# Kernel tuning notes

Hardware: AMD Instinct MI355X
Metric: run time of the kernel (lower is better)

The kernel has to match this reference:

```python
import jax, jax.numpy as jnp
import numpy as np
import math

D_MODEL = 6144
N_HEADS = 48
N_KV_HEADS = 8
HEAD_DIM = D_MODEL // N_HEADS  # 128
ROPE_DIM = HEAD_DIM
ROPE_BASE = 500000.0
CLAMP = 8.0
B, T = 1, 2048


def _apply_rope(x, rope_dim, base):
    # x: [B, n, T, H]; rotate interleaved pairs in first rope_dim dims.
    b, n, t, h = x.shape
    rd = min(rope_dim, h)
    inv = 1.0 / base ** (jnp.arange(0, rd, 2, dtype=jnp.float32) / rd)  # [rd/2]
    pos = jnp.arange(t, dtype=jnp.float32)
    freqs = pos[:, None] * inv[None, :]            # [T, rd/2]
    cos = jnp.cos(freqs)[None, None]               # [1,1,T,rd/2]
    sin = jnp.sin(freqs)[None, None]
    x1 = x[..., :rd].reshape(b, n, t, rd // 2, 2)
    a, b2 = x1[..., 0], x1[..., 1]
    a2 = a * cos - b2 * sin
    b3 = a * sin + b2 * cos
    x1_out = jnp.stack([a2, b3], axis=-1).reshape(b, n, t, rd)
    return jnp.concatenate([x1_out, x[..., rd:]], axis=-1) if rd < h else x1_out


def setup_inputs() -> dict:
    key = jax.random.key(0)
    k1, k2, k3 = jax.random.split(key, 3)
    x = jax.random.normal(k1, (B, T, D_MODEL), dtype=jnp.float32)
    w_qkv = jax.random.normal(k2, (D_MODEL + 2 * N_KV_HEADS * HEAD_DIM, D_MODEL), dtype=jnp.float32) * 0.02
    w_out = jax.random.normal(k3, (D_MODEL, D_MODEL), dtype=jnp.float32) * 0.02
    # additive causal mask: 0 on/below diagonal, -1e9 above
    neg = jnp.full((T, T), -1e9, dtype=jnp.float32)
    causal_mask = jnp.triu(neg, k=1)[None, None]  # [1,1,T,T]
    return {"x": x, "causal_mask": causal_mask, "w_qkv": w_qkv, "w_out": w_out}


def reference(x, causal_mask, w_qkv, w_out):
    b, t, _ = x.shape
    qkv = jnp.einsum('btd,od->bto', x, w_qkv)  # [B,T,8192]
    kv_dim = N_KV_HEADS * HEAD_DIM
    q = qkv[..., :D_MODEL]
    k = qkv[..., D_MODEL:D_MODEL + kv_dim]
    v = qkv[..., D_MODEL + kv_dim:]
    # split heads -> [B, n, T, H]
    q = q.reshape(b, t, N_HEADS, HEAD_DIM).transpose(0, 2, 1, 3)
    k = k.reshape(b, t, N_KV_HEADS, HEAD_DIM).transpose(0, 2, 1, 3)
    v = v.reshape(b, t, N_KV_HEADS, HEAD_DIM).transpose(0, 2, 1, 3)
    q = _apply_rope(q, ROPE_DIM, ROPE_BASE)
    k = _apply_rope(k, ROPE_DIM, ROPE_BASE)
    q = jnp.clip(q, -CLAMP, CLAMP)
    k = jnp.clip(k, -CLAMP, CLAMP)
    v = jnp.clip(v, -CLAMP, CLAMP)
    rep = N_HEADS // N_KV_HEADS
    k = jnp.repeat(k, rep, axis=1)  # GQA repeat_kv -> [B, n_heads, T, H]
    v = jnp.repeat(v, rep, axis=1)
    scale = 1.0 / math.sqrt(HEAD_DIM)
    scores = jnp.einsum('bnqh,bnkh->bnqk', q, k) * scale
    scores = scores + causal_mask
    probs = jax.nn.softmax(scores.astype(jnp.float32), axis=-1).astype(x.dtype)
    attn = jnp.einsum('bnqk,bnkh->bnqh', probs, v)
    attn = attn.transpose(0, 2, 1, 3).reshape(b, t, D_MODEL)
    return jnp.einsum('btd,od->bto', attn, w_out)
```

## Files before the change

### kernel.cpp

```cpp
#include <hip/hip_runtime.h>


typedef __attribute__((ext_vector_type(8))) short bf16x8;
typedef __attribute__((ext_vector_type(4))) float f32x4;

__device__ inline short f2bf(float f) {
  union { float f; unsigned u; } v; v.f = f;
  unsigned r = v.u + 0x7fffu + ((v.u >> 16) & 1u);
  return (short)(r >> 16);
}

__global__ void cvt_bf16(const float* __restrict__ in, short* __restrict__ out, int n8) {
  int i = blockIdx.x * 256 + threadIdx.x;
  if (i >= n8) return;
  const float4* p = (const float4*)in;
  float4 a = p[2 * i], b = p[2 * i + 1];
  bf16x8 r;
  r[0] = f2bf(a.x); r[1] = f2bf(a.y); r[2] = f2bf(a.z); r[3] = f2bf(a.w);
  r[4] = f2bf(b.x); r[5] = f2bf(b.y); r[6] = f2bf(b.z); r[7] = f2bf(b.w);
  *((bf16x8*)out + i) = r;
}

__device__ inline void gload_lds16(const short* g, short* l) {
  __builtin_amdgcn_global_load_lds(
      (const __attribute__((address_space(1))) void*)g,
      (__attribute__((address_space(3))) void*)l, 16, 0, 0);
}

__global__ __launch_bounds__(256) void gemm_bt(const short* __restrict__ A,
                                               const short* __restrict__ B,
                                               float* __restrict__ C,
                                               int M, int N, int K) {
  __shared__ short As[128 * 32];
  __shared__ short Bs[128 * 32];
  int tid = threadIdx.x;
  int wave = tid >> 6, lane = tid & 63;
  int lm = lane & 15, quad = lane >> 4;
  int nwg = gridDim.x * gridDim.y;
  int wg = blockIdx.y * gridDim.x + blockIdx.x;
  int cpx = nwg >> 3;
  int swz = (wg & 7) * cpx + (wg >> 3);
  int bxi = swz % gridDim.x;
  int byi = swz / gridDim.x;
  int bm = byi * 128, bn = bxi * 128;
  int wm = (wave >> 1) * 64, wn = (wave & 1) * 64;
  f32x4 acc[4][4] = {};
  for (int k0 = 0; k0 < K; k0 += 32) {
#pragma unroll
    for (int i = 0; i < 2; ++i) {
      int c = tid + i * 256;
      gload_lds16(A + (size_t)(bm + (c >> 2)) * K + k0 + (c & 3) * 8,
                  As + (i * 256 + wave * 64) * 8);
    }
#pragma unroll
    for (int i = 0; i < 2; ++i) {
      int c = tid + i * 256;
      gload_lds16(B + (size_t)(bn + (c >> 2)) * K + k0 + (c & 3) * 8,
                  Bs + (i * 256 + wave * 64) * 8);
    }
    __syncthreads();
    bf16x8 a[4], b[4];
#pragma unroll
    for (int r = 0; r < 4; ++r)
      a[r] = *(const bf16x8*)(As + (wm + r * 16 + lm) * 32 + quad * 8);
#pragma unroll
    for (int c = 0; c < 4; ++c)
      b[c] = *(const bf16x8*)(Bs + (wn + c * 16 + lm) * 32 + quad * 8);
#pragma unroll
    for (int r = 0; r < 4; ++r)
#pragma unroll
      for (int c = 0; c < 4; ++c)
        acc[r][c] = __builtin_amdgcn_mfma_f32_16x16x32_bf16(a[r], b[c], acc[r][c], 0, 0, 0);
    __syncthreads();
  }
#pragma unroll
  for (int r = 0; r < 4; ++r)
#pragma unroll
    for (int c = 0; c < 4; ++c)
#pragma unroll
      for (int e = 0; e < 4; ++e)
        C[(size_t)(bm + wm + r * 16 + quad * 4 + e) * N + (bn + wn + c * 16 + lm)] =
            acc[r][c][e];
}

__global__ void rope_split(const float* __restrict__ qkv, short* __restrict__ Qb,
                           short* __restrict__ Kb, short* __restrict__ Vtb) {
  int idx = blockIdx.x * 256 + threadIdx.x;
  int t = idx >> 12;
  int p = idx & 4095;
  int o = p * 2;
  float2 ab = *(const float2*)(qkv + (size_t)t * 8192 + o);
  float a = ab.x, b = ab.y;
  if (o < 7168) {
    int d = o & 127;
    float ang = (float)t * exp2f((float)d * (-18.931568569324174f / 128.0f));
    float s, c;
    sincosf(ang, &s, &c);
    float a2 = a * c - b * s;
    float b2 = a * s + b * c;
    a = a2; b = b2;
  }
  a = fminf(8.0f, fmaxf(-8.0f, a));
  b = fminf(8.0f, fmaxf(-8.0f, b));
  short sa = f2bf(a), sb = f2bf(b);
  if (o < 6144) {
    int h = o >> 7, d = o & 127;
    short* q = Qb + (size_t)(h * 2048 + t) * 128 + d;
    q[0] = sa; q[1] = sb;
  } else if (o < 7168) {
    int oo = o - 6144; int h = oo >> 7, d = oo & 127;
    short* k = Kb + (size_t)(h * 2048 + t) * 128 + d;
    k[0] = sa; k[1] = sb;
  } else {
    int oo = o - 7168; int h = oo >> 7, d = oo & 127;
    Vtb[(size_t)(h * 128 + d) * 2048 + t]     = sa;
    Vtb[(size_t)(h * 128 + d + 1) * 2048 + t] = sb;
  }
}

__global__ __launch_bounds__(256) void flash_attn(const short* __restrict__ Q,
                                                  const short* __restrict__ K,
                                                  const short* __restrict__ Vt,
                                                  short* __restrict__ Ob) {
  __shared__ short Ks[64 * 136];
  __shared__ short Vs[128 * 72];
  __shared__ short Ps[4][16 * 72];
  int bid = blockIdx.x;
  int mtile = 31 - (bid / 48);
  int h = bid % 48;
  int hk = h / 6;
  int tid = threadIdx.x, wave = tid >> 6, lane = tid & 63;
  int lm = lane & 15, quad = lane >> 4;
  int qrow0 = mtile * 64 + wave * 16;
  bf16x8 qf[4];
#pragma unroll
  for (int kc = 0; kc < 4; ++kc)
    qf[kc] = *(const bf16x8*)(Q + (size_t)(h * 2048 + qrow0 + lm) * 128 + kc * 32 + quad * 8);
  const short* gk[4]; short* lk[4];
  const short* gv[4]; short* lv[4];
#pragma unroll
  for (int i = 0; i < 4; ++i) {
    int c = tid + i * 256;
    int r = c >> 4, ko = (c & 15) * 8;
    gk[i] = K + (size_t)(hk * 2048 + r) * 128 + ko;
    lk[i] = Ks + r * 136 + ko;
    int d = c >> 3, to = (c & 7) * 8;
    gv[i] = Vt + (size_t)(hk * 128 + d) * 2048 + to;
    lv[i] = Vs + d * 72 + to;
  }
  f32x4 o_acc[8] = {};
  float m_run[4] = {-1e30f, -1e30f, -1e30f, -1e30f};
  float l_run[4] = {0.f, 0.f, 0.f, 0.f};
  const float sc = 0.08838834764831845f;
  int nkv = mtile + 1;
  bf16x8 kst[4], vst[4];
#pragma unroll
  for (int i = 0; i < 4; ++i) {
    kst[i] = *(const bf16x8*)(gk[i]);
    vst[i] = *(const bf16x8*)(gv[i]);
  }
  for (int kb = 0; kb < nkv; ++kb) {
    int kv0 = kb * 64;
    __syncthreads();
#pragma unroll
    for (int i = 0; i < 4; ++i) {
      *(bf16x8*)lk[i] = kst[i];
      *(bf16x8*)lv[i] = vst[i];
    }
    __syncthreads();
    if (kb + 1 < nkv) {
      int kv1 = kv0 + 64;
#pragma unroll
      for (int i = 0; i < 4; ++i) {
        kst[i] = *(const bf16x8*)(gk[i] + (size_t)kv1 * 128);
        vst[i] = *(const bf16x8*)(gv[i] + kv1);
      }
    }
    f32x4 s[4];
    __builtin_amdgcn_s_setprio(1);
#pragma unroll
    for (int ct = 0; ct < 4; ++ct) {
      f32x4 acc = {};
#pragma unroll
      for (int kc = 0; kc < 4; ++kc) {
        bf16x8 bfr = *(const bf16x8*)(Ks + (ct * 16 + lm) * 136 + kc * 32 + quad * 8);
        acc = __builtin_amdgcn_mfma_f32_16x16x32_bf16(qf[kc], bfr, acc, 0, 0, 0);
      }
      s[ct] = acc;
    }
    __builtin_amdgcn_s_setprio(0);
#pragma unroll
    for (int ct = 0; ct < 4; ++ct)
#pragma unroll
      for (int e = 0; e < 4; ++e) s[ct][e] *= sc;
    if (kb == mtile) {
#pragma unroll
      for (int ct = 0; ct < 4; ++ct) {
        int col = kv0 + ct * 16 + lm;
#pragma unroll
        for (int e = 0; e < 4; ++e) {
          int row = qrow0 + quad * 4 + e;
          if (col > row) s[ct][e] = -1e30f;
        }
      }
    }
    float mx[4];
#pragma unroll
    for (int e = 0; e < 4; ++e)
      mx[e] = fmaxf(fmaxf(s[0][e], s[1][e]), fmaxf(s[2][e], s[3][e]));
#pragma unroll
    for (int off = 1; off < 16; off <<= 1)
#pragma unroll
      for (int e = 0; e < 4; ++e) mx[e] = fmaxf(mx[e], __shfl_xor(mx[e], off, 64));
    float alpha[4];
#pragma unroll
    for (int e = 0; e < 4; ++e) {
      float mn = fmaxf(m_run[e], mx[e]);
      alpha[e] = __expf(m_run[e] - mn);
      m_run[e] = mn;
    }
    float rs[4] = {0.f, 0.f, 0.f, 0.f};
#pragma unroll
    for (int ct = 0; ct < 4; ++ct)
#pragma unroll
      for (int e = 0; e < 4; ++e) {
        float pv = __expf(s[ct][e] - m_run[e]);
        s[ct][e] = pv;
        rs[e] += pv;
      }
#pragma unroll
    for (int off = 1; off < 16; off <<= 1)
#pragma unroll
      for (int e = 0; e < 4; ++e) rs[e] += __shfl_xor(rs[e], off, 64);
#pragma unroll
    for (int e = 0; e < 4; ++e) l_run[e] = l_run[e] * alpha[e] + rs[e];
#pragma unroll
    for (int ot = 0; ot < 8; ++ot)
#pragma unroll
      for (int e = 0; e < 4; ++e) o_acc[ot][e] *= alpha[e];
    short* pw = &Ps[wave][0];
#pragma unroll
    for (int ct = 0; ct < 4; ++ct)
#pragma unroll
      for (int e = 0; e < 4; ++e)
        pw[(quad * 4 + e) * 72 + ct * 16 + lm] = f2bf(s[ct][e]);
    __builtin_amdgcn_s_setprio(1);
#pragma unroll
    for (int kc = 0; kc < 2; ++kc) {
      bf16x8 afr = *(const bf16x8*)(pw + lm * 72 + kc * 32 + quad * 8);
#pragma unroll
      for (int ot = 0; ot < 8; ++ot) {
        bf16x8 bfr = *(const bf16x8*)(Vs + (ot * 16 + lm) * 72 + kc * 32 + quad * 8);
        o_acc[ot] = __builtin_amdgcn_mfma_f32_16x16x32_bf16(afr, bfr, o_acc[ot], 0, 0, 0);
      }
    }
    __builtin_amdgcn_s_setprio(0);
  }
#pragma unroll
  for (int ot = 0; ot < 8; ++ot)
#pragma unroll
    for (int e = 0; e < 4; ++e) {
      float v = o_acc[ot][e] / l_run[e];
      Ob[(size_t)(qrow0 + quad * 4 + e) * 6144 + h * 128 + ot * 16 + lm] = f2bf(v);
    }
}

extern "C" void kernel_launch(void* const* d_in, const int* in_sizes, int n_in,
                              void* d_out, int out_size, void* d_ws, size_t ws_size,
                              hipStream_t stream) {
  const float* x     = (const float*)d_in[0];
  const float* w_qkv = (const float*)d_in[2];
  const float* w_out = (const float*)d_in[3];
  float* out = (float*)d_out;

  short* xb    = (short*)d_ws;
  short* wqkvb = xb + (size_t)2048 * 6144;
  short* woutb = wqkvb + (size_t)8192 * 6144;
  float* qkvf  = (float*)(woutb + (size_t)6144 * 6144);
  short* Qb    = (short*)(qkvf + (size_t)2048 * 8192);
  short* Kb    = Qb + (size_t)48 * 2048 * 128;
  short* Vtb   = Kb + (size_t)8 * 2048 * 128;
  short* attnb = Vtb + (size_t)8 * 128 * 2048;

  cvt_bf16<<<(2048 * 6144 / 8) / 256, 256, 0, stream>>>(x, xb, 2048 * 6144 / 8);
  cvt_bf16<<<(8192 * 6144 / 8) / 256, 256, 0, stream>>>(w_qkv, wqkvb, 8192 * 6144 / 8);
  cvt_bf16<<<(6144 * 6144 / 8) / 256, 256, 0, stream>>>(w_out, woutb, 6144 * 6144 / 8);

  gemm_bt<<<dim3(8192 / 128, 2048 / 128), 256, 0, stream>>>(xb, wqkvb, qkvf, 2048, 8192, 6144);

  rope_split<<<(2048 * 4096) / 256, 256, 0, stream>>>(qkvf, Qb, Kb, Vtb);

  flash_attn<<<dim3(1536), 256, 0, stream>>>(Qb, Kb, Vtb, attnb);

  gemm_bt<<<dim3(6144 / 128, 2048 / 128), 256, 0, stream>>>(attnb, woutb, out, 2048, 6144, 6144);
}
```

Before: 1.196 ms.

## Replace GEMM with 256x128 triple-buffered swizzled-LDS pipelined kernel

Swaps the simple 128x128 single-buffered GEMM (K-step 32, two syncthreads per step) for a 256x128 tile kernel with 512 threads, K-step 64 and three LDS buffers. Global-to-LDS loads are issued two tiles ahead, overlapping with the MFMAs. LDS rows are XOR-swizzled to avoid bank conflicts, and s_setprio and sched_barrier pin the schedule. The aim is to hide memory latency and raise MFMA utilisation in both projection GEMMs. The cost is 144KB of dynamic LDS (so 2 blocks/CU is unlikely to fit) and hand-written vmcnt waits that must match the issue order exactly.

```diff
diff --git a/kernel.cpp b/kernel.cpp
--- a/kernel.cpp
+++ b/kernel.cpp
@@ -21,66 +21,147 @@
   *((bf16x8*)out + i) = r;
 }
 
-__device__ inline void gload_lds16(const short* g, short* l) {
+__device__ __forceinline__ void gload_lds16(const short* g, short* l) {
   __builtin_amdgcn_global_load_lds(
       (const __attribute__((address_space(1))) void*)g,
       (__attribute__((address_space(3))) void*)l, 16, 0, 0);
 }
 
-__global__ __launch_bounds__(256) void gemm_bt(const short* __restrict__ A,
-                                               const short* __restrict__ B,
-                                               float* __restrict__ C,
-                                               int M, int N, int K) {
-  __shared__ short As[128 * 32];
-  __shared__ short Bs[128 * 32];
+__device__ __forceinline__ bf16x8 frag_ld(const short* buf, int row, int kb) {
+  int off = row * 128 + (kb ^ ((row & 7) << 4));
+  return *(const bf16x8*)((const char*)buf + off);
+}
+
+__device__ __forceinline__ void pin_barrier() {
+  asm volatile("" ::: "memory");
+  __builtin_amdgcn_sched_barrier(0);
+  __builtin_amdgcn_s_barrier();
+  __builtin_amdgcn_sched_barrier(0);
+}
+
+__device__ __forceinline__ void gemm_tile(
+    int t, int nt, const short* Ac, const short* Bc, short* Asg, short* Bsg,
+    const short* const srcA[4], const int ldsoA[4],
+    const short* const srcB[2], const int ldsoB[2],
+    int wm, int wn, int lm, int quad, f32x4 acc[4][4]) {
+  const bool stage = (t + 2 < nt);
+  const int koff = (t + 2) << 6;
+  bf16x8 a[2][2], b[4][2];
+#pragma unroll
+  for (int fr = 0; fr < 2; ++fr)
+#pragma unroll
+    for (int ks = 0; ks < 2; ++ks)
+      a[fr][ks] = frag_ld(Ac, wm * 64 + fr * 16 + lm, ks * 64 + quad * 16);
+#pragma unroll
+  for (int fc = 0; fc < 4; ++fc)
+#pragma unroll
+    for (int ks = 0; ks < 2; ++ks)
+      b[fc][ks] = frag_ld(Bc, wn * 64 + fc * 16 + lm, ks * 64 + quad * 16);
+  if (stage) {
+#pragma unroll
+    for (int i = 0; i < 4; ++i) gload_lds16(srcA[i] + koff, Asg + ldsoA[i]);
+  }
+  pin_barrier();
+  __builtin_amdgcn_s_setprio(1);
+#pragma unroll
+  for (int fr = 0; fr < 2; ++fr)
+#pragma unroll
+    for (int fc = 0; fc < 4; ++fc) {
+      acc[fr][fc] = __builtin_amdgcn_mfma_f32_16x16x32_bf16(a[fr][0], b[fc][0], acc[fr][fc], 0, 0, 0);
+      acc[fr][fc] = __builtin_amdgcn_mfma_f32_16x16x32_bf16(a[fr][1], b[fc][1], acc[fr][fc], 0, 0, 0);
+    }
+  __builtin_amdgcn_s_setprio(0);
+  pin_barrier();
+  bf16x8 a2[2][2];
+#pragma unroll
+  for (int fr = 0; fr < 2; ++fr)
+#pragma unroll
+    for (int ks = 0; ks < 2; ++ks)
+      a2[fr][ks] = frag_ld(Ac, wm * 64 + (fr + 2) * 16 + lm, ks * 64 + quad * 16);
+  if (stage) {
+#pragma unroll
+    for (int i = 0; i < 2; ++i) gload_lds16(srcB[i] + koff, Bsg + ldsoB[i]);
+    asm volatile("s_waitcnt vmcnt(6)" ::: "memory");
+  } else {
+    asm volatile("s_waitcnt vmcnt(0)" ::: "memory");
+  }
+  pin_barrier();
+  __builtin_amdgcn_s_setprio(1);
+#pragma unroll
+  for (int fr = 0; fr < 2; ++fr)
+#pragma unroll
+    for (int fc = 0; fc < 4; ++fc) {
+      acc[fr + 2][fc] = __builtin_amdgcn_mfma_f32_16x16x32_bf16(a2[fr][0], b[fc][0], acc[fr + 2][fc], 0, 0, 0);
+      acc[fr + 2][fc] = __builtin_amdgcn_mfma_f32_16x16x32_bf16(a2[fr][1], b[fc][1], acc[fr + 2][fc], 0, 0, 0);
+    }
+  __builtin_amdgcn_s_setprio(0);
+  pin_barrier();
+}
+
+__global__ __launch_bounds__(512, 2) void gemm256(const short* __restrict__ A,
+                                                  const short* __restrict__ B,
+                                                  float* __restrict__ C,
+                                                  int M, int N, int K) {
+  extern __shared__ short lds[];
+  short* const A0 = lds;
+  short* const A1 = lds + 16384;
+  short* const A2 = lds + 32768;
+  short* const B0 = lds + 49152;
+  short* const B1 = lds + 57344;
+  short* const B2 = lds + 65536;
   int tid = threadIdx.x;
   int wave = tid >> 6, lane = tid & 63;
   int lm = lane & 15, quad = lane >> 4;
+  int wm = wave >> 1, wn = wave & 1;
   int nwg = gridDim.x * gridDim.y;
   int wg = blockIdx.y * gridDim.x + blockIdx.x;
   int cpx = nwg >> 3;
   int swz = (wg & 7) * cpx + (wg >> 3);
-  int bxi = swz % gridDim.x;
-  int byi = swz / gridDim.x;
-  int bm = byi * 128, bn = bxi * 128;
-  int wm = (wave >> 1) * 64, wn = (wave & 1) * 64;
+  int bn = (swz % gridDim.x) * 128;
+  int bm = (swz / gridDim.x) * 256;
+  int nt = K >> 6;
+  const short* srcA[4]; int ldsoA[4];
+#pragma unroll
+  for (int i = 0; i < 4; ++i) {
+    int c = i * 512 + tid;
+    int row = c >> 3, kc = (c & 7) ^ (row & 7);
+    srcA[i] = A + (size_t)(bm + row) * K + kc * 8;
+    ldsoA[i] = c * 8;
+  }
+  const short* srcB[2]; int ldsoB[2];
+#pragma unroll
+  for (int i = 0; i < 2; ++i) {
+    int c = i * 512 + tid;
+    int row = c >> 3, kc = (c & 7) ^ (row & 7);
+    srcB[i] = B + (size_t)(bn + row) * K + kc * 8;
+    ldsoB[i] = c * 8;
+  }
+#pragma unroll
+  for (int i = 0; i < 4; ++i) gload_lds16(srcA[i], A0 + ldsoA[i]);
+#pragma unroll
+  for (int i = 0; i < 2; ++i) gload_lds16(srcB[i], B0 + ldsoB[i]);
+#pragma unroll
+  for (int i = 0; i < 4; ++i) gload_lds16(srcA[i] + 64, A1 + ldsoA[i]);
+#pragma unroll
+  for (int i = 0; i < 2; ++i) gload_lds16(srcB[i] + 64, B1 + ldsoB[i]);
+  asm volatile("s_waitcnt vmcnt(6)" ::: "memory");
+  __builtin_amdgcn_s_barrier();
+  __builtin_amdgcn_sched_barrier(0);
+
   f32x4 acc[4][4] = {};
-  for (int k0 = 0; k0 < K; k0 += 32) {
-#pragma unroll
-    for (int i = 0; i < 2; ++i) {
-      int c = tid + i * 256;
-      gload_lds16(A + (size_t)(bm + (c >> 2)) * K + k0 + (c & 3) * 8,
-                  As + (i * 256 + wave * 64) * 8);
-    }
-#pragma unroll
-    for (int i = 0; i < 2; ++i) {
-      int c = tid + i * 256;
-      gload_lds16(B + (size_t)(bn + (c >> 2)) * K + k0 + (c & 3) * 8,
-                  Bs + (i * 256 + wave * 64) * 8);
-    }
-    __syncthreads();
-    bf16x8 a[4], b[4];
-#pragma unroll
-    for (int r = 0; r < 4; ++r)
-      a[r] = *(const bf16x8*)(As + (wm + r * 16 + lm) * 32 + quad * 8);
-#pragma unroll
-    for (int c = 0; c < 4; ++c)
-      b[c] = *(const bf16x8*)(Bs + (wn + c * 16 + lm) * 32 + quad * 8);
-#pragma unroll
-    for (int r = 0; r < 4; ++r)
-#pragma unroll
-      for (int c = 0; c < 4; ++c)
-        acc[r][c] = __builtin_amdgcn_mfma_f32_16x16x32_bf16(a[r], b[c], acc[r][c], 0, 0, 0);
-    __syncthreads();
-  }
-#pragma unroll
-  for (int r = 0; r < 4; ++r)
-#pragma unroll
-    for (int c = 0; c < 4; ++c)
+  for (int t = 0; t < nt; t += 3) {
+    gemm_tile(t,     nt, A0, B0, A2, B2, srcA, ldsoA, srcB, ldsoB, wm, wn, lm, quad, acc);
+    gemm_tile(t + 1, nt, A1, B1, A0, B0, srcA, ldsoA, srcB, ldsoB, wm, wn, lm, quad, acc);
+    gemm_tile(t + 2, nt, A2, B2, A1, B1, srcA, ldsoA, srcB, ldsoB, wm, wn, lm, quad, acc);
+  }
+#pragma unroll
+  for (int fr = 0; fr < 4; ++fr)
+#pragma unroll
+    for (int fc = 0; fc < 4; ++fc)
 #pragma unroll
       for (int e = 0; e < 4; ++e)
-        C[(size_t)(bm + wm + r * 16 + quad * 4 + e) * N + (bn + wn + c * 16 + lm)] =
-            acc[r][c][e];
+        C[(size_t)(bm + wm * 64 + fr * 16 + quad * 4 + e) * N + (bn + wn * 64 + fc * 16 + lm)] =
+            acc[fr][fc][e];
 }
 
 __global__ void rope_split(const float* __restrict__ qkv, short* __restrict__ Qb,
@@ -282,15 +363,22 @@
   short* Vtb   = Kb + (size_t)8 * 2048 * 128;
   short* attnb = Vtb + (size_t)8 * 128 * 2048;
 
+  static bool attr_done = false;
+  if (!attr_done) {
+    (void)hipFuncSetAttribute((const void*)gemm256,
+                              hipFuncAttributeMaxDynamicSharedMemorySize, 147456);
+    attr_done = true;
+  }
+
   cvt_bf16<<<(2048 * 6144 / 8) / 256, 256, 0, stream>>>(x, xb, 2048 * 6144 / 8);
   cvt_bf16<<<(8192 * 6144 / 8) / 256, 256, 0, stream>>>(w_qkv, wqkvb, 8192 * 6144 / 8);
   cvt_bf16<<<(6144 * 6144 / 8) / 256, 256, 0, stream>>>(w_out, woutb, 6144 * 6144 / 8);
 
-  gemm_bt<<<dim3(8192 / 128, 2048 / 128), 256, 0, stream>>>(xb, wqkvb, qkvf, 2048, 8192, 6144);
+  gemm256<<<dim3(8192 / 128, 2048 / 256), 512, 147456, stream>>>(xb, wqkvb, qkvf, 2048, 8192, 6144);
 
   rope_split<<<(2048 * 4096) / 256, 256, 0, stream>>>(qkvf, Qb, Kb, Vtb);
 
   flash_attn<<<dim3(1536), 256, 0, stream>>>(Qb, Kb, Vtb, attnb);
 
-  gemm_bt<<<dim3(6144 / 128, 2048 / 128), 256, 0, stream>>>(attnb, woutb, out, 2048, 6144, 6144);
-}
+  gemm256<<<dim3(6144 / 128, 2048 / 256), 512, 147456, stream>>>(attnb, woutb, out, 2048, 6144, 6144);
+}
```

Measured after the change: 1.004 ms. 1.19x faster.

## Replace GEMM with 256x256 double-buffered, XOR-swizzled LDS kernel

Applied to the files above, without the earlier changes.

Swaps the 128x128, K=32 GEMM for a 512-thread kernel computing 256x256 output tiles with a K step of 64. Each wave now holds 8x4 MFMA fragments, which raises data reuse per LDS load. Two LDS buffers let the next tile's global-to-LDS load overlap the current tile's MFMAs. An XOR swizzle on the 16-byte chunks avoids LDS bank conflicts, and setprio raises wave priority around the MFMA bursts. In exchange it needs 128KB of dynamic LDS per block, so only one block fits per CU, and the output projection now has just 192 blocks, fewer than the CU count.

```diff
diff --git a/kernel.cpp b/kernel.cpp
--- a/kernel.cpp
+++ b/kernel.cpp
@@ -21,66 +21,98 @@
   *((bf16x8*)out + i) = r;
 }
 
-__device__ inline void gload_lds16(const short* g, short* l) {
+__device__ __forceinline__ void gload_lds16(const short* g, short* l) {
   __builtin_amdgcn_global_load_lds(
       (const __attribute__((address_space(1))) void*)g,
       (__attribute__((address_space(3))) void*)l, 16, 0, 0);
 }
 
-__global__ __launch_bounds__(256) void gemm_bt(const short* __restrict__ A,
-                                               const short* __restrict__ B,
-                                               float* __restrict__ C,
-                                               int M, int N, int K) {
-  __shared__ short As[128 * 32];
-  __shared__ short Bs[128 * 32];
+__device__ __forceinline__ bf16x8 frag_ld(const short* buf, int row, int kb) {
+  int off = row * 128 + (kb ^ ((row & 7) << 4));
+  return *(const bf16x8*)((const char*)buf + off);
+}
+
+__device__ __forceinline__ void tile256(
+    int t, int nt, const short* Ac, const short* Bc, short* An, short* Bn,
+    const short* const srcA[4], const short* const srcB[4], const int ldso[4],
+    int wm, int wn, int lm, int quad, f32x4 acc[8][4]) {
+  if (t + 1 < nt) {
+    const int koff = (t + 1) << 6;
+#pragma unroll
+    for (int i = 0; i < 4; ++i) {
+      gload_lds16(srcA[i] + koff, An + ldso[i]);
+      gload_lds16(srcB[i] + koff, Bn + ldso[i]);
+    }
+  }
+  __builtin_amdgcn_sched_barrier(0);
+#pragma unroll
+  for (int ks = 0; ks < 2; ++ks) {
+    bf16x8 a[8], b[4];
+    int kb = ks * 64 + quad * 16;
+#pragma unroll
+    for (int fr = 0; fr < 8; ++fr) a[fr] = frag_ld(Ac, wm * 128 + fr * 16 + lm, kb);
+#pragma unroll
+    for (int fc = 0; fc < 4; ++fc) b[fc] = frag_ld(Bc, wn * 64 + fc * 16 + lm, kb);
+    __builtin_amdgcn_s_setprio(1);
+#pragma unroll
+    for (int fr = 0; fr < 8; ++fr)
+#pragma unroll
+      for (int fc = 0; fc < 4; ++fc)
+        acc[fr][fc] = __builtin_amdgcn_mfma_f32_16x16x32_bf16(a[fr], b[fc], acc[fr][fc], 0, 0, 0);
+    __builtin_amdgcn_s_setprio(0);
+  }
+  __syncthreads();
+}
+
+__global__ __launch_bounds__(512, 2) void gemm256(const short* __restrict__ A,
+                                                  const short* __restrict__ B,
+                                                  float* __restrict__ C,
+                                                  int M, int N, int K) {
+  extern __shared__ short lds[];
+  short* const A0 = lds;
+  short* const B0 = lds + 16384;
+  short* const A1 = lds + 32768;
+  short* const B1 = lds + 49152;
   int tid = threadIdx.x;
   int wave = tid >> 6, lane = tid & 63;
   int lm = lane & 15, quad = lane >> 4;
+  int wm = wave >> 2, wn = wave & 3;
   int nwg = gridDim.x * gridDim.y;
   int wg = blockIdx.y * gridDim.x + blockIdx.x;
   int cpx = nwg >> 3;
   int swz = (wg & 7) * cpx + (wg >> 3);
-  int bxi = swz % gridDim.x;
-  int byi = swz / gridDim.x;
-  int bm = byi * 128, bn = bxi * 128;
-  int wm = (wave >> 1) * 64, wn = (wave & 1) * 64;
-  f32x4 acc[4][4] = {};
-  for (int k0 = 0; k0 < K; k0 += 32) {
-#pragma unroll
-    for (int i = 0; i < 2; ++i) {
-      int c = tid + i * 256;
-      gload_lds16(A + (size_t)(bm + (c >> 2)) * K + k0 + (c & 3) * 8,
-                  As + (i * 256 + wave * 64) * 8);
-    }
-#pragma unroll
-    for (int i = 0; i < 2; ++i) {
-      int c = tid + i * 256;
-      gload_lds16(B + (size_t)(bn + (c >> 2)) * K + k0 + (c & 3) * 8,
-                  Bs + (i * 256 + wave * 64) * 8);
-    }
-    __syncthreads();
-    bf16x8 a[4], b[4];
-#pragma unroll
-    for (int r = 0; r < 4; ++r)
-      a[r] = *(const bf16x8*)(As + (wm + r * 16 + lm) * 32 + quad * 8);
-#pragma unroll
-    for (int c = 0; c < 4; ++c)
-      b[c] = *(const bf16x8*)(Bs + (wn + c * 16 + lm) * 32 + quad * 8);
-#pragma unroll
-    for (int r = 0; r < 4; ++r)
-#pragma unroll
-      for (int c = 0; c < 4; ++c)
-        acc[r][c] = __builtin_amdgcn_mfma_f32_16x16x32_bf16(a[r], b[c], acc[r][c], 0, 0, 0);
-    __syncthreads();
-  }
-#pragma unroll
-  for (int r = 0; r < 4; ++r)
-#pragma unroll
-    for (int c = 0; c < 4; ++c)
+  int bn = (swz % gridDim.x) * 256;
+  int bm = (swz / gridDim.x) * 256;
+  int nt = K >> 6;
+  const short* srcA[4]; const short* srcB[4]; int ldso[4];
+#pragma unroll
+  for (int i = 0; i < 4; ++i) {
+    int c = i * 512 + tid;
+    int row = c >> 3, kc = (c & 7) ^ (row & 7);
+    srcA[i] = A + (size_t)(bm + row) * K + kc * 8;
+    srcB[i] = B + (size_t)(bn + row) * K + kc * 8;
+    ldso[i] = c * 8;
+  }
+#pragma unroll
+  for (int i = 0; i < 4; ++i) {
+    gload_lds16(srcA[i], A0 + ldso[i]);
+    gload_lds16(srcB[i], B0 + ldso[i]);
+  }
+  __syncthreads();
+
+  f32x4 acc[8][4] = {};
+  for (int t = 0; t < nt; t += 2) {
+    tile256(t,     nt, A0, B0, A1, B1, srcA, srcB, ldso, wm, wn, lm, quad, acc);
+    tile256(t + 1, nt, A1, B1, A0, B0, srcA, srcB, ldso, wm, wn, lm, quad, acc);
+  }
+#pragma unroll
+  for (int fr = 0; fr < 8; ++fr)
+#pragma unroll
+    for (int fc = 0; fc < 4; ++fc)
 #pragma unroll
       for (int e = 0; e < 4; ++e)
-        C[(size_t)(bm + wm + r * 16 + quad * 4 + e) * N + (bn + wn + c * 16 + lm)] =
-            acc[r][c][e];
+        C[(size_t)(bm + wm * 128 + fr * 16 + quad * 4 + e) * N + (bn + wn * 64 + fc * 16 + lm)] =
+            acc[fr][fc][e];
 }
 
 __global__ void rope_split(const float* __restrict__ qkv, short* __restrict__ Qb,
@@ -282,15 +314,22 @@
   short* Vtb   = Kb + (size_t)8 * 2048 * 128;
   short* attnb = Vtb + (size_t)8 * 128 * 2048;
 
+  static bool attr_done = false;
+  if (!attr_done) {
+    (void)hipFuncSetAttribute((const void*)gemm256,
+                              hipFuncAttributeMaxDynamicSharedMemorySize, 131072);
+    attr_done = true;
+  }
+
   cvt_bf16<<<(2048 * 6144 / 8) / 256, 256, 0, stream>>>(x, xb, 2048 * 6144 / 8);
   cvt_bf16<<<(8192 * 6144 / 8) / 256, 256, 0, stream>>>(w_qkv, wqkvb, 8192 * 6144 / 8);
   cvt_bf16<<<(6144 * 6144 / 8) / 256, 256, 0, stream>>>(w_out, woutb, 6144 * 6144 / 8);
 
-  gemm_bt<<<dim3(8192 / 128, 2048 / 128), 256, 0, stream>>>(xb, wqkvb, qkvf, 2048, 8192, 6144);
+  gemm256<<<dim3(8192 / 256, 2048 / 256), 512, 131072, stream>>>(xb, wqkvb, qkvf, 2048, 8192, 6144);
 
   rope_split<<<(2048 * 4096) / 256, 256, 0, stream>>>(qkvf, Qb, Kb, Vtb);
 
   flash_attn<<<dim3(1536), 256, 0, stream>>>(Qb, Kb, Vtb, attnb);
 
-  gemm_bt<<<dim3(6144 / 128, 2048 / 128), 256, 0, stream>>>(attnb, woutb, out, 2048, 6144, 6144);
-}
+  gemm256<<<dim3(6144 / 256, 2048 / 256), 512, 131072, stream>>>(attnb, woutb, out, 2048, 6144, 6144);
+}
```

Measured after the change: 1.566 ms. +31.0%, slower.
